# Performance work log

Hardware: AMD Instinct MI355X
Metric: run time of the kernel (lower is better)

Reference implementation:

```python
import jax, jax.numpy as jnp
import numpy as np
from functools import partial

INF = 1e10


def _softmin(a, b, c, gamma):
    # soft-min via -gamma * logsumexp(-x/gamma), numerically stable
    z = jnp.stack([a, b, c], axis=0) * (-1.0 / gamma)
    return -gamma * jax.nn.logsumexp(z, axis=0)


def rkd_sdtw(x, gamma):
    """Pairwise soft-DTW distances between all sequence pairs in the batch.

    x: [B, T, D] -> returns [B, B].
    """
    B, T, D = x.shape
    # pairwise squared-euclidean cost: C[a,b,t,s] = ||x[a,t]-x[b,s]||^2
    xn = jnp.sum(x * x, axis=-1)                      # [B, T]
    dot = jnp.einsum('atd,bsd->abts', x, x)           # [B, B, T, T]
    C = xn[:, None, :, None] + xn[None, :, None, :] - 2.0 * dot
    P = B * B
    C = C.reshape(P, T, T)

    idx = jnp.arange(T)

    def shift(r):  # r[i] -> r[i-1], pad INF at i=0
        return jnp.concatenate([jnp.full((P, 1), INF, r.dtype), r[:, :-1]], axis=1)

    def step(carry, d):
        r2, r1 = carry                                # diagonals d-2, d-1: [P, T]
        j = d - idx
        valid = (j >= 0) & (j < T)
        jc = jnp.clip(j, 0, T - 1)
        c_diag = C[:, idx, jc]                        # [P, T] cost on diagonal d
        up = shift(r1)        # R[i-1, j]
        left = r1             # R[i, j-1]
        diag = shift(r2)      # R[i-1, j-1]
        smin = _softmin(up, left, diag, gamma)
        smin = jnp.where(d == 0, 0.0, smin)           # R[0,0] = C[0,0]
        r = jnp.where(valid[None, :], c_diag + smin, INF)
        return (r1, r), None

    init = jnp.full((P, T), INF, C.dtype)
    (_, r_last), _ = jax.lax.scan(step, (init, init), jnp.arange(2 * T - 1))
    return r_last[:, T - 1].reshape(B, B)


def _smooth_l1(pred, target):
    d = pred - target
    ad = jnp.abs(d)
    return jnp.mean(jnp.where(ad < 1.0, 0.5 * d * d, ad - 0.5))


def setup_inputs() -> dict:
    key = jax.random.key(0)
    k1, k2 = jax.random.split(key)
    B, T, D = 32, 96, 128
    student = jax.random.normal(k1, (B, T, D), dtype=jnp.float32)
    teacher = jax.random.normal(k2, (B, T, D), dtype=jnp.float32)
    gamma = jnp.float32(1.0)
    return {"student": student, "teacher": teacher, "gamma": gamma}


def reference(student, teacher, gamma):
    # teacher branch computed under no_grad in torch -> stop_gradient here
    dtw_t = rkd_sdtw(teacher, gamma)
    dtw_t = dtw_t / jnp.mean(dtw_t)
    dtw_t = jax.lax.stop_gradient(dtw_t)

    dtw_s = rkd_sdtw(student, gamma)
    dtw_s = dtw_s / jnp.mean(dtw_s)
    return _smooth_l1(dtw_s, dtw_t)
```

## Files before the change

### kernel.cpp

```cpp
#include <hip/hip_runtime.h>


constexpr int TT = 96;
constexpr int DD = 128;
constexpr int BB = 32;
constexpr int NP = BB * BB;
constexpr int NPAIR = BB * (BB + 1) / 2;
constexpr int NPROB = 2 * NPAIR;
constexpr int CSZ = TT * TT;
constexpr float FINF = 1e10f;
constexpr float LOG2E = 1.4426950408889634f;
constexpr float LN2 = 0.6931471805599453f;

__device__ __forceinline__ int tri_base(int a) {
  return a * BB - (a * (a - 1)) / 2;
}
__device__ __forceinline__ void tri_decode(int pr, int& a, int& b) {
  a = (int)((65.0f - sqrtf(4225.0f - 8.0f * (float)pr)) * 0.5f);
  while (tri_base(a + 1) <= pr) ++a;
  while (tri_base(a) > pr) --a;
  b = a + (pr - tri_base(a));
}
__device__ __forceinline__ int diag_base(int d) {
  return (d <= 95) ? ((d * (d + 1)) >> 1)
                   : 4656 + (((d - 96) * (287 - d)) >> 1);
}
__device__ __forceinline__ float smin2(float u, float lf, float dg) {
  float m = fmaxf(fmaxf(u, lf), dg);
  float s = __builtin_amdgcn_exp2f(u - m) + __builtin_amdgcn_exp2f(lf - m)
          + __builtin_amdgcn_exp2f(dg - m);
  return m + __builtin_amdgcn_logf(s);
}

__global__ void xn_kernel(const float* __restrict__ xs,
                          const float* __restrict__ xt,
                          float* __restrict__ xn) {
  int idx = blockIdx.x * 256 + threadIdx.x;
  if (idx >= 2 * BB * TT) return;
  int which = idx / (BB * TT);
  int row = idx - which * (BB * TT);
  const float* x = which ? xt : xs;
  const float4* xv = reinterpret_cast<const float4*>(x + (size_t)row * DD);
  float acc = 0.f;
#pragma unroll
  for (int k = 0; k < DD / 4; ++k) {
    float4 v = xv[k];
    acc = fmaf(v.x, v.x, acc);
    acc = fmaf(v.y, v.y, acc);
    acc = fmaf(v.z, v.z, acc);
    acc = fmaf(v.w, v.w, acc);
  }
  xn[idx] = acc;
}

__global__ __launch_bounds__(256)
void csq_kernel(const float* __restrict__ xs,
                const float* __restrict__ xt,
                const float* __restrict__ xn,
                const float* __restrict__ gptr,
                float* __restrict__ Cd) {
  __shared__ __align__(16) float Cs[CSZ];
  __shared__ float xna[TT];
  __shared__ float xnb[TT];

  const int pr = blockIdx.x;
  int a, b;
  tri_decode(pr, a, b);
  const int w = blockIdx.y;
  const float* x = w ? xt : xs;
  const float* xnw = xn + w * (BB * TT);
  const float* xa = x + (size_t)a * TT * DD;
  const float* xb = x + (size_t)b * TT * DD;
  const int tid = threadIdx.x;

  if (tid < TT) {
    xna[tid] = xnw[a * TT + tid];
    xnb[tid] = xnw[b * TT + tid];
  }

  constexpr int SROW = 36;
  float* xa_s = Cs;
  float* xb_s = Cs + TT * SROW;

  const int wv = tid >> 6;
  const int lane = tid & 63;
  const int tx = (lane & 7) + (wv & 1) * 8;
  const int ty = (lane >> 3) + (wv >> 1) * 8;
  const int t0 = ty * 6, s0 = tx * 6;

  float acc[6][6];
#pragma unroll
  for (int r = 0; r < 6; ++r)
#pragma unroll
    for (int c = 0; c < 6; ++c) acc[r][c] = 0.f;

  for (int d0 = 0; d0 < DD; d0 += 32) {
    __syncthreads();
    const float4* ga = reinterpret_cast<const float4*>(xa + d0);
    const float4* gb = reinterpret_cast<const float4*>(xb + d0);
    float4* sa = reinterpret_cast<float4*>(xa_s);
    float4* sb = reinterpret_cast<float4*>(xb_s);
#pragma unroll
    for (int it = 0; it < 3; ++it) {
      int idx = tid + it * 256;
      int t = idx >> 3, k4 = idx & 7;
      sa[t * (SROW / 4) + k4] = ga[t * (DD / 4) + k4];
      sb[t * (SROW / 4) + k4] = gb[t * (DD / 4) + k4];
    }
    __syncthreads();
#pragma unroll
    for (int k4 = 0; k4 < 8; ++k4) {
      float4 av4[6], bv4[6];
#pragma unroll
      for (int r = 0; r < 6; ++r)
        av4[r] = reinterpret_cast<const float4*>(xa_s + (t0 + r) * SROW)[k4];
#pragma unroll
      for (int c = 0; c < 6; ++c)
        bv4[c] = reinterpret_cast<const float4*>(xb_s + (s0 + c) * SROW)[k4];
#pragma unroll
      for (int r = 0; r < 6; ++r)
#pragma unroll
        for (int c = 0; c < 6; ++c) {
          acc[r][c] = fmaf(av4[r].x, bv4[c].x, acc[r][c]);
          acc[r][c] = fmaf(av4[r].y, bv4[c].y, acc[r][c]);
          acc[r][c] = fmaf(av4[r].z, bv4[c].z, acc[r][c]);
          acc[r][c] = fmaf(av4[r].w, bv4[c].w, acc[r][c]);
        }
    }
  }
  __syncthreads();
  const float rg2 = -LOG2E / gptr[0];
#pragma unroll
  for (int r = 0; r < 6; ++r) {
    float xr = xna[t0 + r];
#pragma unroll
    for (int c = 0; c < 6; ++c) {
      float cv = xr + xnb[s0 + c] - 2.0f * acc[r][c];
      Cs[(t0 + r) * TT + (s0 + c)] = cv * rg2;
    }
  }
  __syncthreads();

  const size_t qb = (size_t)(w * NPAIR + pr) * CSZ;
  for (int d = wv; d < 2 * TT - 1; d += 4) {
    int s = d <= 95 ? 0 : d - 95;
    int len = d <= 95 ? d + 1 : 191 - d;
    int base = diag_base(d);
    if (lane < len) {
      int i = s + lane;
      Cd[qb + base + lane] = Cs[i * TT + (d - i)];
    }
    if (len > 64 && lane < len - 64) {
      int i = s + 64 + lane;
      Cd[qb + base + 64 + lane] = Cs[i * TT + (d - i)];
    }
  }
}

#define STEP_RISE(d, qa, qb) do {                                        \
    float cA = qa, cB = qb;                                              \
    int dn = (d) + 8;                                                    \
    if (dn <= 190) {                                                     \
      int nb = diag_base(dn);                                            \
      qa = cb[nb + l]; qb = cb[nb + 64 + l];                             \
    }                                                                    \
    float rA1 = __shfl(A1, lm1), rB1 = __shfl(B1, lm1);                  \
    float upA = l0 ? NEGI : rA1;                                         \
    float dgA = l0 ? NEGI : pA1;                                         \
    float upB = l0 ? rA1 : rB1;                                          \
    float dgB = l0 ? pA1 : pB1;                                          \
    float nA = cA + smin2(upA, A1, dgA);                                 \
    float nB = cB + smin2(upB, B1, dgB);                                 \
    A2 = A1; B2 = B1;                                                    \
    A1 = (l < (d) + 1) ? nA : NEGI;                                      \
    B1 = (64 + l < (d) + 1) ? nB : NEGI;                                 \
    pA1 = rA1; pB1 = rB1;                                                \
  } while (0)

#define STEP_FALL(d, qa, qb) do {                                        \
    float cA = qa, cB = qb;                                              \
    int dn = (d) + 8;                                                    \
    if (dn <= 190) {                                                     \
      int nb = diag_base(dn);                                            \
      qa = cb[nb + l]; qb = cb[nb + 64 + l];                             \
    }                                                                    \
    float rA1 = __shfl(A1, lp1), rB1 = __shfl(B1, lp1);                  \
    float lfA = l63 ? rB1 : rA1;                                         \
    float lfB = rB1;                                                     \
    float dgA = l63 ? pB1 : pA1;                                         \
    float dgB = pB1;                                                     \
    float nA = cA + smin2(A1, lfA, dgA);                                 \
    float nB = cB + smin2(B1, lfB, dgB);                                 \
    A2 = A1; B2 = B1;                                                    \
    int len = 191 - (d);                                                 \
    A1 = (l < len) ? nA : NEGI;                                          \
    B1 = (64 + l < len) ? nB : NEGI;                                     \
    pA1 = rA1; pB1 = rB1;                                                \
  } while (0)

__global__ __launch_bounds__(64)
void dp_kernel(const float* __restrict__ Cd,
               const float* __restrict__ gptr,
               float* __restrict__ dtw) {
  const int q = blockIdx.x;
  const int l = threadIdx.x;
  const float gamma = gptr[0];
  const float rg2 = -LOG2E / gamma;
  const float NEGI = FINF * rg2;
  const float* __restrict__ cb = Cd + (size_t)q * CSZ;
  const int lp1 = (l + 1) & 63, lm1 = (l + 63) & 63;
  const bool l0 = (l == 0), l63 = (l == 63);

  float q0A, q0B, q1A, q1B, q2A, q2B, q3A, q3B;
  float q4A, q4B, q5A, q5B, q6A, q6B, q7A, q7B;
  {
    int b1 = diag_base(1), b2 = diag_base(2), b3 = diag_base(3), b4 = diag_base(4);
    int b5 = diag_base(5), b6 = diag_base(6), b7 = diag_base(7), b8 = diag_base(8);
    q0A = cb[b1 + l]; q0B = cb[b1 + 64 + l];
    q1A = cb[b2 + l]; q1B = cb[b2 + 64 + l];
    q2A = cb[b3 + l]; q2B = cb[b3 + 64 + l];
    q3A = cb[b4 + l]; q3B = cb[b4 + 64 + l];
    q4A = cb[b5 + l]; q4B = cb[b5 + 64 + l];
    q5A = cb[b6 + l]; q5B = cb[b6 + 64 + l];
    q6A = cb[b7 + l]; q6B = cb[b7 + 64 + l];
    q7A = cb[b8 + l]; q7B = cb[b8 + 64 + l];
  }

  float A1 = l0 ? cb[0] : NEGI;
  float B1 = NEGI, A2 = NEGI, B2 = NEGI;
  float pA1 = NEGI, pB1 = NEGI;

  for (int g = 0; g < 11; ++g) {
    int d = 1 + g * 8;
    STEP_RISE(d,     q0A, q0B);
    STEP_RISE(d + 1, q1A, q1B);
    STEP_RISE(d + 2, q2A, q2B);
    STEP_RISE(d + 3, q3A, q3B);
    STEP_RISE(d + 4, q4A, q4B);
    STEP_RISE(d + 5, q5A, q5B);
    STEP_RISE(d + 6, q6A, q6B);
    STEP_RISE(d + 7, q7A, q7B);
  }
  STEP_RISE(89, q0A, q0B);
  STEP_RISE(90, q1A, q1B);
  STEP_RISE(91, q2A, q2B);
  STEP_RISE(92, q3A, q3B);
  STEP_RISE(93, q4A, q4B);
  STEP_RISE(94, q5A, q5B);
  STEP_RISE(95, q6A, q6B);

  {
    float cA = q7A, cB = q7B;
    int nb = diag_base(104);
    q7A = cb[nb + l]; q7B = cb[nb + 64 + l];
    float rA1 = __shfl(A1, lp1), rB1 = __shfl(B1, lp1);
    float lfA = l63 ? rB1 : rA1;
    float lfB = rB1;
    float nA = cA + smin2(A1, lfA, A2);
    float nB = cB + smin2(B1, lfB, B2);
    A2 = A1; B2 = B1;
    A1 = (l < 95) ? nA : NEGI;
    B1 = (64 + l < 95) ? nB : NEGI;
    pA1 = rA1; pB1 = rB1;
  }

  for (int g = 0; g < 11; ++g) {
    int d = 97 + g * 8;
    STEP_FALL(d,     q0A, q0B);
    STEP_FALL(d + 1, q1A, q1B);
    STEP_FALL(d + 2, q2A, q2B);
    STEP_FALL(d + 3, q3A, q3B);
    STEP_FALL(d + 4, q4A, q4B);
    STEP_FALL(d + 5, q5A, q5B);
    STEP_FALL(d + 6, q6A, q6B);
    STEP_FALL(d + 7, q7A, q7B);
  }
  STEP_FALL(185, q0A, q0B);
  STEP_FALL(186, q1A, q1B);
  STEP_FALL(187, q2A, q2B);
  STEP_FALL(188, q3A, q3B);
  STEP_FALL(189, q4A, q4B);
  STEP_FALL(190, q5A, q5B);

  if (l0) {
    int w = q >= NPAIR ? 1 : 0;
    int pr = q - w * NPAIR;
    int a, b;
    tri_decode(pr, a, b);
    float v = A1 * (-gamma * LN2);
    dtw[w * NP + a * BB + b] = v;
    dtw[w * NP + b * BB + a] = v;
  }
}

__global__ __launch_bounds__(256)
void sdtw_fused_kernel(const float* __restrict__ xs,
                       const float* __restrict__ xt,
                       const float* __restrict__ xn,
                       const float* __restrict__ gptr,
                       float* __restrict__ dtw) {
  __shared__ __align__(16) float Cs[TT * TT];
  __shared__ float xna[TT];
  __shared__ float xnb[TT];

  const int pr = blockIdx.x;
  int a, b;
  tri_decode(pr, a, b);
  const int w = blockIdx.y;
  const float* x = w ? xt : xs;
  const float* xnw = xn + w * (BB * TT);
  const float* xa = x + (size_t)a * TT * DD;
  const float* xb = x + (size_t)b * TT * DD;
  const int tid = threadIdx.x;

  if (tid < TT) {
    xna[tid] = xnw[a * TT + tid];
    xnb[tid] = xnw[b * TT + tid];
  }
  constexpr int SROW = 36;
  float* xa_s = Cs;
  float* xb_s = Cs + TT * SROW;
  const int wv = tid >> 6;
  const int lane = tid & 63;
  const int tx = (lane & 7) + (wv & 1) * 8;
  const int ty = (lane >> 3) + (wv >> 1) * 8;
  const int t0 = ty * 6, s0 = tx * 6;
  float acc[6][6];
#pragma unroll
  for (int r = 0; r < 6; ++r)
#pragma unroll
    for (int c = 0; c < 6; ++c) acc[r][c] = 0.f;
  for (int d0 = 0; d0 < DD; d0 += 32) {
    __syncthreads();
    const float4* ga = reinterpret_cast<const float4*>(xa + d0);
    const float4* gb = reinterpret_cast<const float4*>(xb + d0);
    float4* sa = reinterpret_cast<float4*>(xa_s);
    float4* sb = reinterpret_cast<float4*>(xb_s);
#pragma unroll
    for (int it = 0; it < 3; ++it) {
      int idx = tid + it * 256;
      int t = idx >> 3, k4 = idx & 7;
      sa[t * (SROW / 4) + k4] = ga[t * (DD / 4) + k4];
      sb[t * (SROW / 4) + k4] = gb[t * (DD / 4) + k4];
    }
    __syncthreads();
#pragma unroll
    for (int k4 = 0; k4 < 8; ++k4) {
      float4 av4[6], bv4[6];
#pragma unroll
      for (int r = 0; r < 6; ++r)
        av4[r] = reinterpret_cast<const float4*>(xa_s + (t0 + r) * SROW)[k4];
#pragma unroll
      for (int c = 0; c < 6; ++c)
        bv4[c] = reinterpret_cast<const float4*>(xb_s + (s0 + c) * SROW)[k4];
#pragma unroll
      for (int r = 0; r < 6; ++r)
#pragma unroll
        for (int c = 0; c < 6; ++c) {
          acc[r][c] = fmaf(av4[r].x, bv4[c].x, acc[r][c]);
          acc[r][c] = fmaf(av4[r].y, bv4[c].y, acc[r][c]);
          acc[r][c] = fmaf(av4[r].z, bv4[c].z, acc[r][c]);
          acc[r][c] = fmaf(av4[r].w, bv4[c].w, acc[r][c]);
        }
    }
  }
  __syncthreads();
#pragma unroll
  for (int r = 0; r < 6; ++r) {
    float xr = xna[t0 + r];
#pragma unroll
    for (int c = 0; c < 6; ++c)
      Cs[(t0 + r) * TT + (s0 + c)] = xr + xnb[s0 + c] - 2.0f * acc[r][c];
  }
  __syncthreads();
  if (tid >= 64) return;

  const float gamma = gptr[0];
  const float rg = -1.0f / gamma;
  const int lm1 = (lane + 63) & 63;
  float A1 = FINF, B1 = FINF, A2 = FINF, B2 = FINF;
  for (int d = 0; d < 2 * TT - 1; ++d) {
    int jA = d - lane;
    bool vA = (jA >= 0) && (jA < TT);
    float cA = Cs[vA ? lane * TT + jA : 0];
    int iB = 64 + lane;
    int jB = d - iB;
    bool vB = (lane < 32) && (jB >= 0) && (jB < TT);
    float cB = Cs[vB ? iB * TT + jB : 0];
    float rA1 = __shfl(A1, lm1);
    float rB1 = __shfl(B1, lm1);
    float rA2 = __shfl(A2, lm1);
    float rB2 = __shfl(B2, lm1);
    const bool l0 = (lane == 0);
    float upA = l0 ? FINF : rA1;
    float dgA = l0 ? FINF : rA2;
    float upB = l0 ? rA1 : rB1;
    float dgB = l0 ? rA2 : rB2;
    float z0 = upA * rg, z1 = A1 * rg, z2 = dgA * rg;
    float m = fmaxf(fmaxf(z0, z1), z2);
    float s = expf(z0 - m) + expf(z1 - m) + expf(z2 - m);
    float sminA = -gamma * (m + logf(s));
    if (d == 0) sminA = 0.f;
    float y0 = upB * rg, y1 = B1 * rg, y2 = dgB * rg;
    float mb = fmaxf(fmaxf(y0, y1), y2);
    float sb2 = expf(y0 - mb) + expf(y1 - mb) + expf(y2 - mb);
    float sminB = -gamma * (mb + logf(sb2));
    float nA = vA ? cA + sminA : FINF;
    float nB = vB ? cB + sminB : FINF;
    A2 = A1; B2 = B1; A1 = nA; B1 = nB;
  }
  if (lane == 31) {
    float v = B1;
    dtw[w * NP + a * BB + b] = v;
    dtw[w * NP + b * BB + a] = v;
  }
}

__global__ void reduce_kernel(const float* __restrict__ dtw,
                              float* __restrict__ out) {
  __shared__ double sh[256];
  const int tid = threadIdx.x;
  double ss = 0, st = 0;
  for (int k = tid; k < NP; k += 256) {
    ss += (double)dtw[k];
    st += (double)dtw[NP + k];
  }
  sh[tid] = ss; __syncthreads();
  for (int o = 128; o > 0; o >>= 1) { if (tid < o) sh[tid] += sh[tid + o]; __syncthreads(); }
  double sum_s = sh[0]; __syncthreads();
  sh[tid] = st; __syncthreads();
  for (int o = 128; o > 0; o >>= 1) { if (tid < o) sh[tid] += sh[tid + o]; __syncthreads(); }
  double sum_t = sh[0]; __syncthreads();

  float mean_s = (float)(sum_s / NP);
  float mean_t = (float)(sum_t / NP);

  double acc = 0;
  for (int k = tid; k < NP; k += 256) {
    float pred = dtw[k] / mean_s;
    float targ = dtw[NP + k] / mean_t;
    float d = pred - targ;
    float ad = fabsf(d);
    float v = ad < 1.f ? 0.5f * d * d : ad - 0.5f;
    acc += (double)v;
  }
  sh[tid] = acc; __syncthreads();
  for (int o = 128; o > 0; o >>= 1) { if (tid < o) sh[tid] += sh[tid + o]; __syncthreads(); }
  if (tid == 0) out[0] = (float)(sh[0] / NP);
}

extern "C" void kernel_launch(void* const* d_in, const int* in_sizes, int n_in,
                              void* d_out, int out_size, void* d_ws, size_t ws_size,
                              hipStream_t stream) {
  const float* student = (const float*)d_in[0];
  const float* teacher = (const float*)d_in[1];
  const float* gamma   = (const float*)d_in[2];
  float* ws = (float*)d_ws;

  const size_t cd_floats = (size_t)NPROB * CSZ;
  const size_t need = (cd_floats + 2 * NP + 2 * BB * TT) * sizeof(float);

  if (ws_size >= need) {
    float* Cd  = ws;
    float* dtw = ws + cd_floats;
    float* xnb = dtw + 2 * NP;
    xn_kernel<<<24, 256, 0, stream>>>(student, teacher, xnb);
    csq_kernel<<<dim3(NPAIR, 2), 256, 0, stream>>>(student, teacher, xnb, gamma, Cd);
    dp_kernel<<<NPROB, 64, 0, stream>>>(Cd, gamma, dtw);
    reduce_kernel<<<1, 256, 0, stream>>>(dtw, (float*)d_out);
  } else {
    float* dtw = ws;
    float* xnb = ws + 2 * NP;
    xn_kernel<<<24, 256, 0, stream>>>(student, teacher, xnb);
    sdtw_fused_kernel<<<dim3(NPAIR, 2), 256, 0, stream>>>(student, teacher, xnb, gamma, dtw);
    reduce_kernel<<<1, 256, 0, stream>>>(dtw, (float*)d_out);
  }
}
```

Before: 108.6 us.

## Pair two b-sequences per cost block and skip inactive upper-half DP lanes

Each cost-matrix block now computes two (a,b) pairs that share the same a-sequence tile, reusing the A loads. It writes the cost directly in diagonal-major order into shared memory, so the store-out reads contiguous data. In the DP kernel, the second 64-lane half is only loaded, shuffled and updated when its diagonal range is active, and the step loops are unrolled via a switch so diagonal indices are compile-time constants. This trades more registers (two 6x6 accumulators) and fewer blocks for less redundant load and ALU work.

```diff
diff --git a/kernel.cpp b/kernel.cpp
--- a/kernel.cpp
+++ b/kernel.cpp
@@ -7,6 +7,7 @@
 constexpr int NP = BB * BB;
 constexpr int NPAIR = BB * (BB + 1) / 2;
 constexpr int NPROB = 2 * NPAIR;
+constexpr int NGRP = 272;
 constexpr int CSZ = TT * TT;
 constexpr float FINF = 1e10f;
 constexpr float LOG2E = 1.4426950408889634f;
@@ -59,28 +60,29 @@
                 const float* __restrict__ xn,
                 const float* __restrict__ gptr,
                 float* __restrict__ Cd) {
-  __shared__ __align__(16) float Cs[CSZ];
+  __shared__ __align__(16) float BUF[3 * TT * 36];
   __shared__ float xna[TT];
-  __shared__ float xnb[TT];
-
-  const int pr = blockIdx.x;
-  int a, b;
-  tri_decode(pr, a, b);
+  __shared__ float xnb0[TT];
+  __shared__ float xnb1[TT];
+
+  int g = blockIdx.x, a = 0;
+  for (;;) { int cnt = (BB - a + 1) >> 1; if (g < cnt) break; g -= cnt; ++a; }
+  const int b0 = a + 2 * g;
+  const int b1 = (b0 + 1 < BB) ? b0 + 1 : b0;
+
   const int w = blockIdx.y;
   const float* x = w ? xt : xs;
   const float* xnw = xn + w * (BB * TT);
-  const float* xa = x + (size_t)a * TT * DD;
-  const float* xb = x + (size_t)b * TT * DD;
+  const float* xa  = x + (size_t)a  * TT * DD;
+  const float* xb0 = x + (size_t)b0 * TT * DD;
+  const float* xb1 = x + (size_t)b1 * TT * DD;
   const int tid = threadIdx.x;
 
   if (tid < TT) {
-    xna[tid] = xnw[a * TT + tid];
-    xnb[tid] = xnw[b * TT + tid];
-  }
-
-  constexpr int SROW = 36;
-  float* xa_s = Cs;
-  float* xb_s = Cs + TT * SROW;
+    xna[tid]  = xnw[a  * TT + tid];
+    xnb0[tid] = xnw[b0 * TT + tid];
+    xnb1[tid] = xnw[b1 * TT + tid];
+  }
 
   const int wv = tid >> 6;
   const int lane = tid & 63;
@@ -88,114 +90,155 @@
   const int ty = (lane >> 3) + (wv >> 1) * 8;
   const int t0 = ty * 6, s0 = tx * 6;
 
-  float acc[6][6];
+  float acc0[6][6], acc1[6][6];
 #pragma unroll
   for (int r = 0; r < 6; ++r)
 #pragma unroll
-    for (int c = 0; c < 6; ++c) acc[r][c] = 0.f;
+    for (int c = 0; c < 6; ++c) { acc0[r][c] = 0.f; acc1[r][c] = 0.f; }
 
   for (int d0 = 0; d0 < DD; d0 += 32) {
     __syncthreads();
-    const float4* ga = reinterpret_cast<const float4*>(xa + d0);
-    const float4* gb = reinterpret_cast<const float4*>(xb + d0);
-    float4* sa = reinterpret_cast<float4*>(xa_s);
-    float4* sb = reinterpret_cast<float4*>(xb_s);
+    const float4* ga  = reinterpret_cast<const float4*>(xa  + d0);
+    const float4* gb0 = reinterpret_cast<const float4*>(xb0 + d0);
+    const float4* gb1 = reinterpret_cast<const float4*>(xb1 + d0);
+    float4* s4 = reinterpret_cast<float4*>(BUF);
 #pragma unroll
     for (int it = 0; it < 3; ++it) {
       int idx = tid + it * 256;
       int t = idx >> 3, k4 = idx & 7;
-      sa[t * (SROW / 4) + k4] = ga[t * (DD / 4) + k4];
-      sb[t * (SROW / 4) + k4] = gb[t * (DD / 4) + k4];
+      s4[t * 9 + k4]        = ga [t * 32 + k4];
+      s4[864 + t * 9 + k4]  = gb0[t * 32 + k4];
+      s4[1728 + t * 9 + k4] = gb1[t * 32 + k4];
     }
     __syncthreads();
+    const float4* B4 = reinterpret_cast<const float4*>(BUF);
 #pragma unroll
     for (int k4 = 0; k4 < 8; ++k4) {
-      float4 av4[6], bv4[6];
+      float4 av[6], bv[6];
+#pragma unroll
+      for (int r = 0; r < 6; ++r) av[r] = B4[(t0 + r) * 9 + k4];
+#pragma unroll
+      for (int c = 0; c < 6; ++c) bv[c] = B4[864 + (s0 + c) * 9 + k4];
 #pragma unroll
       for (int r = 0; r < 6; ++r)
-        av4[r] = reinterpret_cast<const float4*>(xa_s + (t0 + r) * SROW)[k4];
-#pragma unroll
-      for (int c = 0; c < 6; ++c)
-        bv4[c] = reinterpret_cast<const float4*>(xb_s + (s0 + c) * SROW)[k4];
+#pragma unroll
+        for (int c = 0; c < 6; ++c) {
+          acc0[r][c] = fmaf(av[r].x, bv[c].x, acc0[r][c]);
+          acc0[r][c] = fmaf(av[r].y, bv[c].y, acc0[r][c]);
+          acc0[r][c] = fmaf(av[r].z, bv[c].z, acc0[r][c]);
+          acc0[r][c] = fmaf(av[r].w, bv[c].w, acc0[r][c]);
+        }
+#pragma unroll
+      for (int c = 0; c < 6; ++c) bv[c] = B4[1728 + (s0 + c) * 9 + k4];
 #pragma unroll
       for (int r = 0; r < 6; ++r)
 #pragma unroll
         for (int c = 0; c < 6; ++c) {
-          acc[r][c] = fmaf(av4[r].x, bv4[c].x, acc[r][c]);
-          acc[r][c] = fmaf(av4[r].y, bv4[c].y, acc[r][c]);
-          acc[r][c] = fmaf(av4[r].z, bv4[c].z, acc[r][c]);
-          acc[r][c] = fmaf(av4[r].w, bv4[c].w, acc[r][c]);
+          acc1[r][c] = fmaf(av[r].x, bv[c].x, acc1[r][c]);
+          acc1[r][c] = fmaf(av[r].y, bv[c].y, acc1[r][c]);
+          acc1[r][c] = fmaf(av[r].z, bv[c].z, acc1[r][c]);
+          acc1[r][c] = fmaf(av[r].w, bv[c].w, acc1[r][c]);
         }
     }
   }
+
+  const float rg2 = -LOG2E / gptr[0];
+  float* Cs = BUF;
+  const int pr0 = tri_base(a) + (b0 - a);
+
   __syncthreads();
-  const float rg2 = -LOG2E / gptr[0];
 #pragma unroll
   for (int r = 0; r < 6; ++r) {
-    float xr = xna[t0 + r];
+    const int i = t0 + r;
+    float xr = xna[i];
 #pragma unroll
     for (int c = 0; c < 6; ++c) {
-      float cv = xr + xnb[s0 + c] - 2.0f * acc[r][c];
-      Cs[(t0 + r) * TT + (s0 + c)] = cv * rg2;
+      const int j = s0 + c;
+      float cv = xr + xnb0[j] - 2.0f * acc0[r][c];
+      const int d = i + j;
+      const int pos = (d <= 95) ? i : i - (d - 95);
+      Cs[diag_base(d) + pos] = cv * rg2;
     }
   }
   __syncthreads();
-
-  const size_t qb = (size_t)(w * NPAIR + pr) * CSZ;
-  for (int d = wv; d < 2 * TT - 1; d += 4) {
-    int s = d <= 95 ? 0 : d - 95;
-    int len = d <= 95 ? d + 1 : 191 - d;
-    int base = diag_base(d);
-    if (lane < len) {
-      int i = s + lane;
-      Cd[qb + base + lane] = Cs[i * TT + (d - i)];
-    }
-    if (len > 64 && lane < len - 64) {
-      int i = s + 64 + lane;
-      Cd[qb + base + 64 + lane] = Cs[i * TT + (d - i)];
+  {
+    const size_t qb = (size_t)(w * NPAIR + pr0) * CSZ;
+    for (int d = wv; d < 2 * TT - 1; d += 4) {
+      int len = d <= 95 ? d + 1 : 191 - d;
+      int base = diag_base(d);
+      if (lane < len)                 Cd[qb + base + lane]      = Cs[base + lane];
+      if (len > 64 && lane < len - 64) Cd[qb + base + 64 + lane] = Cs[base + 64 + lane];
+    }
+  }
+
+  if (b1 > b0) {
+    __syncthreads();
+#pragma unroll
+    for (int r = 0; r < 6; ++r) {
+      const int i = t0 + r;
+      float xr = xna[i];
+#pragma unroll
+      for (int c = 0; c < 6; ++c) {
+        const int j = s0 + c;
+        float cv = xr + xnb1[j] - 2.0f * acc1[r][c];
+        const int d = i + j;
+        const int pos = (d <= 95) ? i : i - (d - 95);
+        Cs[diag_base(d) + pos] = cv * rg2;
+      }
+    }
+    __syncthreads();
+    const size_t qb = (size_t)(w * NPAIR + pr0 + 1) * CSZ;
+    for (int d = wv; d < 2 * TT - 1; d += 4) {
+      int len = d <= 95 ? d + 1 : 191 - d;
+      int base = diag_base(d);
+      if (lane < len)                 Cd[qb + base + lane]      = Cs[base + lane];
+      if (len > 64 && lane < len - 64) Cd[qb + base + 64 + lane] = Cs[base + 64 + lane];
     }
   }
 }
 
 #define STEP_RISE(d, qa, qb) do {                                        \
-    float cA = qa, cB = qb;                                              \
-    int dn = (d) + 8;                                                    \
-    if (dn <= 190) {                                                     \
-      int nb = diag_base(dn);                                            \
-      qa = cb[nb + l]; qb = cb[nb + 64 + l];                             \
-    }                                                                    \
-    float rA1 = __shfl(A1, lm1), rB1 = __shfl(B1, lm1);                  \
+    float cA = qa;                                                       \
+    { int dn = (d) + 8;                                                  \
+      if (dn <= 190) { int nb = diag_base(dn); qa = cb[nb + l]; }        \
+      if (dn <= 190 && dn >= 64) { int nb = diag_base(dn); qb = cb[nb + 64 + l]; } } \
+    float rA1 = __shfl(A1, lm1);                                         \
     float upA = l0 ? NEGI : rA1;                                         \
     float dgA = l0 ? NEGI : pA1;                                         \
-    float upB = l0 ? rA1 : rB1;                                          \
-    float dgB = l0 ? pA1 : pB1;                                          \
     float nA = cA + smin2(upA, A1, dgA);                                 \
-    float nB = cB + smin2(upB, B1, dgB);                                 \
-    A2 = A1; B2 = B1;                                                    \
+    if ((d) >= 64) {                                                     \
+      float cB = qb;                                                     \
+      float rB1 = __shfl(B1, lm1);                                       \
+      float upB = l0 ? rA1 : rB1;                                        \
+      float dgB = l0 ? pA1 : pB1;                                        \
+      float nB = cB + smin2(upB, B1, dgB);                               \
+      B2 = B1;                                                           \
+      B1 = (64 + l < (d) + 1) ? nB : NEGI;                               \
+      pB1 = rB1;                                                         \
+    }                                                                    \
+    A2 = A1;                                                             \
     A1 = (l < (d) + 1) ? nA : NEGI;                                      \
-    B1 = (64 + l < (d) + 1) ? nB : NEGI;                                 \
-    pA1 = rA1; pB1 = rB1;                                                \
+    pA1 = rA1;                                                           \
   } while (0)
 
 #define STEP_FALL(d, qa, qb) do {                                        \
-    float cA = qa, cB = qb;                                              \
-    int dn = (d) + 8;                                                    \
-    if (dn <= 190) {                                                     \
-      int nb = diag_base(dn);                                            \
-      qa = cb[nb + l]; qb = cb[nb + 64 + l];                             \
+    float cA = qa;                                                       \
+    { int dn = (d) + 8;                                                  \
+      if (dn <= 190) { int nb = diag_base(dn); qa = cb[nb + l]; }        \
+      if (dn <= 128) { int nb = diag_base(dn); qb = cb[nb + 64 + l]; } } \
+    float rA1 = __shfl(A1, lp1);                                         \
+    float rB1 = ((d) <= 128) ? __shfl(B1, lp1) : NEGI;                   \
+    float lfA = l63 ? rB1 : rA1;                                         \
+    float dgA = l63 ? pB1 : pA1;                                         \
+    float nA = cA + smin2(A1, lfA, dgA);                                 \
+    if ((d) <= 128) {                                                    \
+      float cB = qb;                                                     \
+      float nB = cB + smin2(B1, rB1, pB1);                               \
+      B1 = (64 + l < 191 - (d)) ? nB : NEGI;                             \
+      pB1 = rB1;                                                         \
     }                                                                    \
-    float rA1 = __shfl(A1, lp1), rB1 = __shfl(B1, lp1);                  \
-    float lfA = l63 ? rB1 : rA1;                                         \
-    float lfB = rB1;                                                     \
-    float dgA = l63 ? pB1 : pA1;                                         \
-    float dgB = pB1;                                                     \
-    float nA = cA + smin2(A1, lfA, dgA);                                 \
-    float nB = cB + smin2(B1, lfB, dgB);                                 \
-    A2 = A1; B2 = B1;                                                    \
-    int len = 191 - (d);                                                 \
-    A1 = (l < len) ? nA : NEGI;                                          \
-    B1 = (64 + l < len) ? nB : NEGI;                                     \
-    pA1 = rA1; pB1 = rB1;                                                \
+    A1 = (l < 191 - (d)) ? nA : NEGI;                                    \
+    pA1 = rA1;                                                           \
   } while (0)
 
 __global__ __launch_bounds__(64)
@@ -213,17 +256,12 @@
 
   float q0A, q0B, q1A, q1B, q2A, q2B, q3A, q3B;
   float q4A, q4B, q5A, q5B, q6A, q6B, q7A, q7B;
+  q0B = q1B = q2B = q3B = q4B = q5B = q6B = q7B = NEGI;
   {
     int b1 = diag_base(1), b2 = diag_base(2), b3 = diag_base(3), b4 = diag_base(4);
     int b5 = diag_base(5), b6 = diag_base(6), b7 = diag_base(7), b8 = diag_base(8);
-    q0A = cb[b1 + l]; q0B = cb[b1 + 64 + l];
-    q1A = cb[b2 + l]; q1B = cb[b2 + 64 + l];
-    q2A = cb[b3 + l]; q2B = cb[b3 + 64 + l];
-    q3A = cb[b4 + l]; q3B = cb[b4 + 64 + l];
-    q4A = cb[b5 + l]; q4B = cb[b5 + 64 + l];
-    q5A = cb[b6 + l]; q5B = cb[b6 + 64 + l];
-    q6A = cb[b7 + l]; q6B = cb[b7 + 64 + l];
-    q7A = cb[b8 + l]; q7B = cb[b8 + 64 + l];
+    q0A = cb[b1 + l]; q1A = cb[b2 + l]; q2A = cb[b3 + l]; q3A = cb[b4 + l];
+    q4A = cb[b5 + l]; q5A = cb[b6 + l]; q6A = cb[b7 + l]; q7A = cb[b8 + l];
   }
 
   float A1 = l0 ? cb[0] : NEGI;
@@ -232,14 +270,30 @@
 
   for (int g = 0; g < 11; ++g) {
     int d = 1 + g * 8;
-    STEP_RISE(d,     q0A, q0B);
-    STEP_RISE(d + 1, q1A, q1B);
-    STEP_RISE(d + 2, q2A, q2B);
-    STEP_RISE(d + 3, q3A, q3B);
-    STEP_RISE(d + 4, q4A, q4B);
-    STEP_RISE(d + 5, q5A, q5B);
-    STEP_RISE(d + 6, q6A, q6B);
-    STEP_RISE(d + 7, q7A, q7B);
+    switch (d) {
+      case 1:  STEP_RISE(1,q0A,q0B);  STEP_RISE(2,q1A,q1B);  STEP_RISE(3,q2A,q2B);  STEP_RISE(4,q3A,q3B);
+               STEP_RISE(5,q4A,q4B);  STEP_RISE(6,q5A,q5B);  STEP_RISE(7,q6A,q6B);  STEP_RISE(8,q7A,q7B);  break;
+      case 9:  STEP_RISE(9,q0A,q0B);  STEP_RISE(10,q1A,q1B); STEP_RISE(11,q2A,q2B); STEP_RISE(12,q3A,q3B);
+               STEP_RISE(13,q4A,q4B); STEP_RISE(14,q5A,q5B); STEP_RISE(15,q6A,q6B); STEP_RISE(16,q7A,q7B); break;
+      case 17: STEP_RISE(17,q0A,q0B); STEP_RISE(18,q1A,q1B); STEP_RISE(19,q2A,q2B); STEP_RISE(20,q3A,q3B);
+               STEP_RISE(21,q4A,q4B); STEP_RISE(22,q5A,q5B); STEP_RISE(23,q6A,q6B); STEP_RISE(24,q7A,q7B); break;
+      case 25: STEP_RISE(25,q0A,q0B); STEP_RISE(26,q1A,q1B); STEP_RISE(27,q2A,q2B); STEP_RISE(28,q3A,q3B);
+               STEP_RISE(29,q4A,q4B); STEP_RISE(30,q5A,q5B); STEP_RISE(31,q6A,q6B); STEP_RISE(32,q7A,q7B); break;
+      case 33: STEP_RISE(33,q0A,q0B); STEP_RISE(34,q1A,q1B); STEP_RISE(35,q2A,q2B); STEP_RISE(36,q3A,q3B);
+               STEP_RISE(37,q4A,q4B); STEP_RISE(38,q5A,q5B); STEP_RISE(39,q6A,q6B); STEP_RISE(40,q7A,q7B); break;
+      case 41: STEP_RISE(41,q0A,q0B); STEP_RISE(42,q1A,q1B); STEP_RISE(43,q2A,q2B); STEP_RISE(44,q3A,q3B);
+               STEP_RISE(45,q4A,q4B); STEP_RISE(46,q5A,q5B); STEP_RISE(47,q6A,q6B); STEP_RISE(48,q7A,q7B); break;
+      case 49: STEP_RISE(49,q0A,q0B); STEP_RISE(50,q1A,q1B); STEP_RISE(51,q2A,q2B); STEP_RISE(52,q3A,q3B);
+               STEP_RISE(53,q4A,q4B); STEP_RISE(54,q5A,q5B); STEP_RISE(55,q6A,q6B); STEP_RISE(56,q7A,q7B); break;
+      case 57: STEP_RISE(57,q0A,q0B); STEP_RISE(58,q1A,q1B); STEP_RISE(59,q2A,q2B); STEP_RISE(60,q3A,q3B);
+               STEP_RISE(61,q4A,q4B); STEP_RISE(62,q5A,q5B); STEP_RISE(63,q6A,q6B); STEP_RISE(64,q7A,q7B); break;
+      case 65: STEP_RISE(65,q0A,q0B); STEP_RISE(66,q1A,q1B); STEP_RISE(67,q2A,q2B); STEP_RISE(68,q3A,q3B);
+               STEP_RISE(69,q4A,q4B); STEP_RISE(70,q5A,q5B); STEP_RISE(71,q6A,q6B); STEP_RISE(72,q7A,q7B); break;
+      case 73: STEP_RISE(73,q0A,q0B); STEP_RISE(74,q1A,q1B); STEP_RISE(75,q2A,q2B); STEP_RISE(76,q3A,q3B);
+               STEP_RISE(77,q4A,q4B); STEP_RISE(78,q5A,q5B); STEP_RISE(79,q6A,q6B); STEP_RISE(80,q7A,q7B); break;
+      default: STEP_RISE(81,q0A,q0B); STEP_RISE(82,q1A,q1B); STEP_RISE(83,q2A,q2B); STEP_RISE(84,q3A,q3B);
+               STEP_RISE(85,q4A,q4B); STEP_RISE(86,q5A,q5B); STEP_RISE(87,q6A,q6B); STEP_RISE(88,q7A,q7B); break;
+    }
   }
   STEP_RISE(89, q0A, q0B);
   STEP_RISE(90, q1A, q1B);
@@ -266,14 +320,30 @@
 
   for (int g = 0; g < 11; ++g) {
     int d = 97 + g * 8;
-    STEP_FALL(d,     q0A, q0B);
-    STEP_FALL(d + 1, q1A, q1B);
-    STEP_FALL(d + 2, q2A, q2B);
-    STEP_FALL(d + 3, q3A, q3B);
-    STEP_FALL(d + 4, q4A, q4B);
-    STEP_FALL(d + 5, q5A, q5B);
-    STEP_FALL(d + 6, q6A, q6B);
-    STEP_FALL(d + 7, q7A, q7B);
+    switch (d) {
+      case 97:  STEP_FALL(97,q0A,q0B);  STEP_FALL(98,q1A,q1B);  STEP_FALL(99,q2A,q2B);  STEP_FALL(100,q3A,q3B);
+                STEP_FALL(101,q4A,q4B); STEP_FALL(102,q5A,q5B); STEP_FALL(103,q6A,q6B); STEP_FALL(104,q7A,q7B); break;
+      case 105: STEP_FALL(105,q0A,q0B); STEP_FALL(106,q1A,q1B); STEP_FALL(107,q2A,q2B); STEP_FALL(108,q3A,q3B);
+                STEP_FALL(109,q4A,q4B); STEP_FALL(110,q5A,q5B); STEP_FALL(111,q6A,q6B); STEP_FALL(112,q7A,q7B); break;
+      case 113: STEP_FALL(113,q0A,q0B); STEP_FALL(114,q1A,q1B); STEP_FALL(115,q2A,q2B); STEP_FALL(116,q3A,q3B);
+                STEP_FALL(117,q4A,q4B); STEP_FALL(118,q5A,q5B); STEP_FALL(119,q6A,q6B); STEP_FALL(120,q7A,q7B); break;
+      case 121: STEP_FALL(121,q0A,q0B); STEP_FALL(122,q1A,q1B); STEP_FALL(123,q2A,q2B); STEP_FALL(124,q3A,q3B);
+                STEP_FALL(125,q4A,q4B); STEP_FALL(126,q5A,q5B); STEP_FALL(127,q6A,q6B); STEP_FALL(128,q7A,q7B); break;
+      case 129: STEP_FALL(129,q0A,q0B); STEP_FALL(130,q1A,q1B); STEP_FALL(131,q2A,q2B); STEP_FALL(132,q3A,q3B);
+                STEP_FALL(133,q4A,q4B); STEP_FALL(134,q5A,q5B); STEP_FALL(135,q6A,q6B); STEP_FALL(136,q7A,q7B); break;
+      case 137: STEP_FALL(137,q0A,q0B); STEP_FALL(138,q1A,q1B); STEP_FALL(139,q2A,q2B); STEP_FALL(140,q3A,q3B);
+                STEP_FALL(141,q4A,q4B); STEP_FALL(142,q5A,q5B); STEP_FALL(143,q6A,q6B); STEP_FALL(144,q7A,q7B); break;
+      case 145: STEP_FALL(145,q0A,q0B); STEP_FALL(146,q1A,q1B); STEP_FALL(147,q2A,q2B); STEP_FALL(148,q3A,q3B);
+                STEP_FALL(149,q4A,q4B); STEP_FALL(150,q5A,q5B); STEP_FALL(151,q6A,q6B); STEP_FALL(152,q7A,q7B); break;
+      case 153: STEP_FALL(153,q0A,q0B); STEP_FALL(154,q1A,q1B); STEP_FALL(155,q2A,q2B); STEP_FALL(156,q3A,q3B);
+                STEP_FALL(157,q4A,q4B); STEP_FALL(158,q5A,q5B); STEP_FALL(159,q6A,q6B); STEP_FALL(160,q7A,q7B); break;
+      case 161: STEP_FALL(161,q0A,q0B); STEP_FALL(162,q1A,q1B); STEP_FALL(163,q2A,q2B); STEP_FALL(164,q3A,q3B);
+                STEP_FALL(165,q4A,q4B); STEP_FALL(166,q5A,q5B); STEP_FALL(167,q6A,q6B); STEP_FALL(168,q7A,q7B); break;
+      case 169: STEP_FALL(169,q0A,q0B); STEP_FALL(170,q1A,q1B); STEP_FALL(171,q2A,q2B); STEP_FALL(172,q3A,q3B);
+                STEP_FALL(173,q4A,q4B); STEP_FALL(174,q5A,q5B); STEP_FALL(175,q6A,q6B); STEP_FALL(176,q7A,q7B); break;
+      default:  STEP_FALL(177,q0A,q0B); STEP_FALL(178,q1A,q1B); STEP_FALL(179,q2A,q2B); STEP_FALL(180,q3A,q3B);
+                STEP_FALL(181,q4A,q4B); STEP_FALL(182,q5A,q5B); STEP_FALL(183,q6A,q6B); STEP_FALL(184,q7A,q7B); break;
+    }
   }
   STEP_FALL(185, q0A, q0B);
   STEP_FALL(186, q1A, q1B);
@@ -465,7 +535,7 @@
     float* dtw = ws + cd_floats;
     float* xnb = dtw + 2 * NP;
     xn_kernel<<<24, 256, 0, stream>>>(student, teacher, xnb);
-    csq_kernel<<<dim3(NPAIR, 2), 256, 0, stream>>>(student, teacher, xnb, gamma, Cd);
+    csq_kernel<<<dim3(NGRP, 2), 256, 0, stream>>>(student, teacher, xnb, gamma, Cd);
     dp_kernel<<<NPROB, 64, 0, stream>>>(Cd, gamma, dtw);
     reduce_kernel<<<1, 256, 0, stream>>>(dtw, (float*)d_out);
   } else {
```

New measurement: 150.4 us. +38.5%, slower.
